# Optimization experiments

Hardware: AMD Instinct MI355X
Metric: run time of the kernel (lower is better)

The kernel has to match this reference:

```python
import jax, jax.numpy as jnp
import numpy as np

N = 100000
E = 1000000
P = 1000000
HID = 128
ROLE_VOCAB = 8
ROLE_DIM = 16
IDX_VOCAB = 1024
IDX_DIM = 8
FEAT = 14
IN_DIM = FEAT + IDX_DIM + ROLE_DIM  # 38


def setup_inputs() -> dict:
    key = jax.random.key(0)
    ks = jax.random.split(key, 20)
    s = 0.02
    return {
        "block_features": jax.random.normal(ks[0], (N, FEAT), jnp.float32),
        "role_ids": jax.random.randint(ks[1], (N,), 0, ROLE_VOCAB),
        "b2b_src": jax.random.randint(ks[2], (E,), 0, N),
        "b2b_dst": jax.random.randint(ks[3], (E,), 0, N),
        "b2b_w": jax.random.uniform(ks[4], (E,), jnp.float32),
        "p2b_block": jax.random.randint(ks[5], (P,), 0, N),
        "p2b_w": jax.random.uniform(ks[6], (P,), jnp.float32),
        "role_emb": jax.random.normal(ks[7], (ROLE_VOCAB, ROLE_DIM), jnp.float32),
        "idx_emb": jax.random.normal(ks[8], (IDX_VOCAB, IDX_DIM), jnp.float32),
        "W1": jax.random.normal(ks[9], (IN_DIM, HID), jnp.float32) * s,
        "b1": jnp.zeros((HID,), jnp.float32),
        "W2": jax.random.normal(ks[10], (HID, HID), jnp.float32) * s,
        "b2": jnp.zeros((HID,), jnp.float32),
        "M1": jax.random.normal(ks[11], (HID, HID), jnp.float32) * s,
        "mb1": jnp.zeros((HID,), jnp.float32),
        "M2": jax.random.normal(ks[12], (HID, HID), jnp.float32) * s,
        "mb2": jnp.zeros((HID,), jnp.float32),
        "ln_g": jnp.ones((HID,), jnp.float32),
        "ln_b": jnp.zeros((HID,), jnp.float32),
    }


def _layernorm(x, g, b, eps=1e-5):
    mu = jnp.mean(x, axis=-1, keepdims=True)
    var = jnp.mean(jnp.square(x - mu), axis=-1, keepdims=True)
    return (x - mu) * jax.lax.rsqrt(var + eps) * g + b


def reference(block_features, role_ids, b2b_src, b2b_dst, b2b_w, p2b_block, p2b_w,
              role_emb, idx_emb, W1, b1, W2, b2, M1, mb1, M2, mb2, ln_g, ln_b):
    n = block_features.shape[0]
    # embeddings + input MLP
    re = role_emb[role_ids]                                  # [N, 16]
    ie = idx_emb[jnp.arange(n) % IDX_VOCAB]                  # [N, 8]
    x = jnp.concatenate([block_features, re, ie], axis=-1)   # [N, 38]
    h = jax.nn.relu(x @ W1 + b1)
    emb = jax.nn.relu(h @ W2 + b2)                           # [N, HID]
    # b2b: symmetric weighted scatter-add of neighbor embeddings
    agg = jnp.zeros_like(emb)
    agg = agg.at[b2b_src].add(emb[b2b_dst] * b2b_w[:, None])
    agg = agg.at[b2b_dst].add(emb[b2b_src] * b2b_w[:, None])
    # p2b: agg[j] += emb[j] * w  ==  emb * (sum of pin weights per block)
    pw = jnp.zeros((n,), emb.dtype).at[p2b_block].add(p2b_w)
    agg = agg + emb * pw[:, None]
    # message MLP + residual + LayerNorm
    m = jax.nn.relu(agg @ M1 + mb1) @ M2 + mb2
    block_embeddings = _layernorm(emb + m, ln_g, ln_b)
    graph_embedding = jnp.mean(block_embeddings, axis=0)
    return block_embeddings, graph_embedding
```

## Files before the change

kernel.cpp:

```cpp
#include <hip/hip_runtime.h>

#define FEAT 14
#define ROLE_DIM 16
#define IDX_DIM 8
#define IN_DIM 38
#define HID 128
#define IDX_VOCAB 1024
#define BINN 128
#define NBINS_MAX 800
#define TILE_E 2048
#define CAPT 16
#define SCAP 64
#define SORT_CAP 4096

typedef __attribute__((ext_vector_type(8))) short short8;
typedef __attribute__((ext_vector_type(4))) float f32x4;
typedef __attribute__((ext_vector_type(2))) float f32x2;

__device__ __forceinline__ ushort f2bf(float f) {
    uint u = __float_as_uint(f);
    return (ushort)((u + 0x7FFFu + ((u >> 16) & 1u)) >> 16);
}
__device__ __forceinline__ float bf2f(ushort h) {
    return __uint_as_float((uint)h << 16);
}
__device__ __forceinline__ uchar f2fp8(float f) {
    return (uchar)(__builtin_amdgcn_cvt_pk_fp8_f32(f, f, 0, false) & 0xff);
}

__global__ void k_prep(const float* __restrict__ W1, const float* __restrict__ W2,
                       const float* __restrict__ M1, const float* __restrict__ M2,
                       ushort* __restrict__ W1t, ushort* __restrict__ W2t,
                       ushort* __restrict__ M1t, ushort* __restrict__ M2t)
{
    int t = blockIdx.x * 256 + threadIdx.x;
    if (t < 8192) {
        int c = t >> 6, k = t & 63;
        W1t[t] = (k < IN_DIM) ? f2bf(W1[k * HID + c]) : (ushort)0;
    } else if (t < 24576) {
        int u = t - 8192; int c = u >> 7, k = u & 127;
        W2t[u] = f2bf(W2[k * HID + c]);
    } else if (t < 40960) {
        int u = t - 24576; int c = u >> 7, k = u & 127;
        M1t[u] = f2bf(M1[k * HID + c]);
    } else if (t < 57344) {
        int u = t - 40960; int c = u >> 7, k = u & 127;
        M2t[u] = f2bf(M2[k * HID + c]);
    }
}

#define LDSA 32768

__global__ __launch_bounds__(256) void k_embed_mlp(
    const float* __restrict__ feat, const int* __restrict__ role_ids,
    const float* __restrict__ role_emb, const float* __restrict__ idx_emb,
    const ushort* __restrict__ W1t, const float* __restrict__ b1,
    const ushort* __restrict__ W2t, const float* __restrict__ b2,
    ushort* __restrict__ embh, uchar* __restrict__ embf8, int N)
{
    __shared__ char lds[49152];
    const int tid = threadIdx.x;
    const int w = tid >> 6, l = tid & 63;
    const int li = l & 15, hi = l >> 4;
    const int base = blockIdx.x * 64;

    for (int c = 0; c < 4; ++c) {
        int idx = c * 256 + tid;
        int col = idx >> 3, ch = idx & 7;
        uint4 v = *(const uint4*)(W1t + col * 64 + ch * 8);
        *(uint4*)(lds + col * 256 + ((ch * 16) ^ ((col & 7) << 4))) = v;
    }
    {
        int row = tid >> 2, kq = (tid & 3) * 16;
        int gr = base + row; if (gr >= N) gr = N - 1;
        int rid = role_ids[gr];
        float xv[16];
        #pragma unroll
        for (int j = 0; j < 16; ++j) {
            int k = kq + j;
            float v = 0.0f;
            if (k < FEAT)                 v = feat[gr * FEAT + k];
            else if (k < FEAT + ROLE_DIM) v = role_emb[rid * ROLE_DIM + (k - FEAT)];
            else if (k < IN_DIM)          v = idx_emb[(gr & (IDX_VOCAB - 1)) * IDX_DIM + (k - FEAT - ROLE_DIM)];
            xv[j] = v;
        }
        uint p[8];
        #pragma unroll
        for (int j = 0; j < 8; ++j)
            p[j] = (uint)f2bf(xv[2 * j]) | ((uint)f2bf(xv[2 * j + 1]) << 16);
        char* db = lds + LDSA + row * 256;
        int sw = (row & 7) << 4;
        *(uint4*)(db + ((kq * 2) ^ sw))      = make_uint4(p[0], p[1], p[2], p[3]);
        *(uint4*)(db + ((kq * 2 + 16) ^ sw)) = make_uint4(p[4], p[5], p[6], p[7]);
    }
    __syncthreads();

    f32x4 C[8];
    #pragma unroll
    for (int ct = 0; ct < 8; ++ct) C[ct] = (f32x4){0.f, 0.f, 0.f, 0.f};
    {
        const int arow = w * 16 + li;
        const int asw = (arow & 7) << 4;
        #pragma unroll
        for (int ks = 0; ks < 2; ++ks) {
            short8 a = *(short8*)(lds + LDSA + arow * 256 + ((ks * 64 + hi * 16) ^ asw));
            #pragma unroll
            for (int ct = 0; ct < 8; ++ct) {
                int bcol = ct * 16 + li;
                short8 b = *(short8*)(lds + bcol * 256 + ((ks * 64 + hi * 16) ^ ((bcol & 7) << 4)));
                C[ct] = __builtin_amdgcn_mfma_f32_16x16x32_bf16(a, b, C[ct], 0, 0, 0);
            }
        }
    }
    __syncthreads();

    #pragma unroll
    for (int ct = 0; ct < 8; ++ct) {
        int col = ct * 16 + li;
        float bv = b1[col];
        #pragma unroll
        for (int r = 0; r < 4; ++r) {
            int hrow = w * 16 + hi * 4 + r;
            float h = fmaxf(C[ct][r] + bv, 0.0f);
            *(ushort*)(lds + LDSA + hrow * 256 + ((col * 2) ^ ((hrow & 7) << 4))) = f2bf(h);
        }
    }
    for (int c = 0; c < 8; ++c) {
        int idx = c * 256 + tid;
        int col = idx >> 4, ch = idx & 15;
        uint4 v = *(const uint4*)(W2t + col * 128 + ch * 8);
        *(uint4*)(lds + col * 256 + ((ch * 16) ^ ((col & 7) << 4))) = v;
    }
    __syncthreads();

    f32x4 C2[8];
    #pragma unroll
    for (int ct = 0; ct < 8; ++ct) C2[ct] = (f32x4){0.f, 0.f, 0.f, 0.f};
    {
        const int arow = w * 16 + li;
        const int asw = (arow & 7) << 4;
        #pragma unroll
        for (int ks = 0; ks < 4; ++ks) {
            short8 a = *(short8*)(lds + LDSA + arow * 256 + ((ks * 64 + hi * 16) ^ asw));
            #pragma unroll
            for (int ct = 0; ct < 8; ++ct) {
                int bcol = ct * 16 + li;
                short8 b = *(short8*)(lds + bcol * 256 + ((ks * 64 + hi * 16) ^ ((bcol & 7) << 4)));
                C2[ct] = __builtin_amdgcn_mfma_f32_16x16x32_bf16(a, b, C2[ct], 0, 0, 0);
            }
        }
    }

    #pragma unroll
    for (int ct = 0; ct < 8; ++ct) {
        int col = ct * 16 + li;
        float bv = b2[col];
        #pragma unroll
        for (int r = 0; r < 4; ++r) {
            int gr = base + w * 16 + hi * 4 + r;
            if (gr < N) {
                float o = fmaxf(C2[ct][r] + bv, 0.0f);
                embh[(size_t)gr * 128 + col] = f2bf(o);
                embf8[(size_t)gr * 128 + col] = f2fp8(o);
            }
        }
    }
}

__global__ __launch_bounds__(1024) void k_binp(
    const int* __restrict__ src, const int* __restrict__ dst,
    const float* __restrict__ w, uint* __restrict__ staged,
    int* __restrict__ cnt,
    const int* __restrict__ pb, const float* __restrict__ pv,
    float* __restrict__ pw,
    int E, int P, int nbins, int chunk, int chunkP)
{
    __shared__ uint buf[NBINS_MAX * CAPT];
    __shared__ int curT[NBINS_MAX];
    __shared__ int segCur[NBINS_MAX];
    const int tid = threadIdx.x;
    const int blk = blockIdx.x;
    for (int i = tid; i < nbins; i += 1024) { curT[i] = 0; segCur[i] = 0; }
    __syncthreads();

    const int lo = blk * chunk;
    const int hiE = (lo + chunk) < E ? (lo + chunk) : E;
    for (int t0 = lo; t0 < hiE; t0 += TILE_E) {
        int t1 = t0 + TILE_E; if (t1 > hiE) t1 = hiE;
        for (int i = t0 + tid; i < t1; i += 1024) {
            int s = src[i], d = dst[i];
            uint q = (uint)(w[i] * 255.0f + 0.5f);
            int bs = s >> 7;
            uint es = ((uint)(s & 127) << 25) | ((uint)d << 8) | q;
            int ps = atomicAdd(&curT[bs], 1);
            if (ps < CAPT) buf[bs * CAPT + ps] = es;
            else { int gp = segCur[bs] + ps;
                   if (gp < SCAP) staged[((size_t)bs * 256 + blk) * SCAP + gp] = es; }
            int bd = d >> 7;
            uint ed = ((uint)(d & 127) << 25) | ((uint)s << 8) | q;
            int pd = atomicAdd(&curT[bd], 1);
            if (pd < CAPT) buf[bd * CAPT + pd] = ed;
            else { int gp = segCur[bd] + pd;
                   if (gp < SCAP) staged[((size_t)bd * 256 + blk) * SCAP + gp] = ed; }
        }
        __syncthreads();
        for (int b = tid; b < nbins; b += 1024) {
            int tot = curT[b];
            int base = segCur[b];
            int k = tot < CAPT ? tot : CAPT;
            if (base + k > SCAP) { k = SCAP - base; if (k < 0) k = 0; }
            uint* dp = staged + ((size_t)b * 256 + blk) * SCAP + base;
            for (int i = 0; i < k; ++i) dp[i] = buf[b * CAPT + i];
            segCur[b] = base + tot;
            curT[b] = 0;
        }
        __syncthreads();
    }
    for (int i = tid; i < nbins; i += 1024)
        cnt[blk * nbins + i] = segCur[i] < SCAP ? segCur[i] : SCAP;

    int loP = blk * chunkP;
    int hiP = loP + chunkP; if (hiP > P) hiP = P;
    for (int i = loP + tid; i < hiP; i += 1024)
        atomicAdd(&pw[pb[i]], pv[i]);
}

#define AREG 32768
#define WSUM 65536

__global__ __launch_bounds__(256) void k_agg_mlp(
    const uint* __restrict__ staged, const int* __restrict__ cnt,
    const ushort* __restrict__ embh, const uchar* __restrict__ embf8,
    const float* __restrict__ pw,
    const ushort* __restrict__ M1t, const ushort* __restrict__ M2t,
    const float* __restrict__ mb1, const float* __restrict__ mb2,
    const float* __restrict__ ln_g, const float* __restrict__ ln_b,
    float* __restrict__ out, float* __restrict__ gsum, int N, int nbins)
{
    __shared__ char lds[67584];
    uint* sorted  = (uint*)lds;
    int*  hist    = (int*)(lds + 16384);
    int*  startL  = (int*)(lds + 16384 + 512);
    int*  curL    = (int*)(lds + 16384 + 1024);
    int*  sc      = (int*)(lds + 16384 + 1536);

    const int tid = threadIdx.x;
    const int b = blockIdx.x;
    const int baseNode = b << 7;
    const int w = tid >> 6, l = tid & 63;
    const int li = l & 15, hi = l >> 4;

    if (tid < BINN) hist[tid] = 0;
    __syncthreads();

    const int c = cnt[tid * nbins + b];
    const uint* sp = staged + ((size_t)b * 256 + tid) * SCAP;
    for (int k = 0; k < c; ++k)
        atomicAdd(&hist[sp[k] >> 25], 1);
    __syncthreads();

    int v = (tid < BINN) ? hist[tid] : 0;
    if (tid < BINN) sc[tid] = v;
    __syncthreads();
    for (int off = 1; off < BINN; off <<= 1) {
        int u = (tid < BINN && tid >= off) ? sc[tid - off] : 0;
        __syncthreads();
        if (tid < BINN) sc[tid] += u;
        __syncthreads();
    }
    if (tid < BINN) {
        startL[tid] = sc[tid] - v;
        curL[tid]   = sc[tid] - v;
    }
    __syncthreads();

    for (int k = 0; k < c; ++k) {
        uint e = sp[k];
        int pos = atomicAdd(&curL[e >> 25], 1);
        if (pos < SORT_CAP) sorted[pos] = e;
    }
    __syncthreads();

    {
        const int g  = tid >> 3;
        const int cg = tid & 7;
        const int c0 = cg * 16;
        for (int h = 0; h < 4; ++h) {
            int nl = h * 32 + g;
            int node = baseNode + nl;
            uint p[8];
            if (node < N) {
                float acc[16];
                float pwn = pw[node];
                const uint4* r = (const uint4*)(embh + ((size_t)node << 7) + c0);
                uint4 u0 = r[0], u1 = r[1];
                uint uu[8] = {u0.x, u0.y, u0.z, u0.w, u1.x, u1.y, u1.z, u1.w};
                #pragma unroll
                for (int j = 0; j < 8; ++j) {
                    acc[2*j]   = __uint_as_float(uu[j] << 16) * pwn;
                    acc[2*j+1] = __uint_as_float(uu[j] & 0xffff0000u) * pwn;
                }
                const int st = startL[nl], deg = hist[nl];
                #pragma unroll 4
                for (int i = 0; i < deg; ++i) {
                    uint en = sorted[st + i];
                    int nb   = (int)((en >> 8) & 0x1FFFFu);
                    float wt = (float)(en & 255u) * (1.0f / 255.0f);
                    uint4 q = *(const uint4*)(embf8 + ((size_t)nb << 7) + c0);
                    uint qq[4] = {q.x, q.y, q.z, q.w};
                    #pragma unroll
                    for (int j = 0; j < 4; ++j) {
                        f32x2 lo = __builtin_amdgcn_cvt_pk_f32_fp8(qq[j], false);
                        f32x2 hi2 = __builtin_amdgcn_cvt_pk_f32_fp8(qq[j], true);
                        acc[4*j+0] = fmaf(lo.x,  wt, acc[4*j+0]);
                        acc[4*j+1] = fmaf(lo.y,  wt, acc[4*j+1]);
                        acc[4*j+2] = fmaf(hi2.x, wt, acc[4*j+2]);
                        acc[4*j+3] = fmaf(hi2.y, wt, acc[4*j+3]);
                    }
                }
                #pragma unroll
                for (int j = 0; j < 8; ++j)
                    p[j] = (uint)f2bf(acc[2*j]) | ((uint)f2bf(acc[2*j+1]) << 16);
            } else {
                #pragma unroll
                for (int j = 0; j < 8; ++j) p[j] = 0;
            }
            char* db = lds + AREG + nl * 256;
            int sw = (nl & 7) << 4;
            *(uint4*)(db + ((c0 * 2) ^ sw))      = make_uint4(p[0], p[1], p[2], p[3]);
            *(uint4*)(db + ((c0 * 2 + 16) ^ sw)) = make_uint4(p[4], p[5], p[6], p[7]);
        }
    }
    __syncthreads();

    for (int cc = 0; cc < 8; ++cc) {
        int idx = cc * 256 + tid;
        int col = idx >> 4, ch = idx & 15;
        uint4 vv = *(const uint4*)(M1t + col * 128 + ch * 8);
        *(uint4*)(lds + col * 256 + ((ch * 16) ^ ((col & 7) << 4))) = vv;
    }
    __syncthreads();

    #pragma unroll
    for (int h2 = 0; h2 < 2; ++h2) {
        f32x4 C1[8];
        #pragma unroll
        for (int ct = 0; ct < 8; ++ct) C1[ct] = (f32x4){0.f, 0.f, 0.f, 0.f};
        const int arow = h2 * 64 + w * 16 + li;
        const int asw = (arow & 7) << 4;
        #pragma unroll
        for (int ks = 0; ks < 4; ++ks) {
            short8 a = *(short8*)(lds + AREG + arow * 256 + ((ks * 64 + hi * 16) ^ asw));
            #pragma unroll
            for (int ct = 0; ct < 8; ++ct) {
                int bcol = ct * 16 + li;
                short8 bb = *(short8*)(lds + bcol * 256 + ((ks * 64 + hi * 16) ^ ((bcol & 7) << 4)));
                C1[ct] = __builtin_amdgcn_mfma_f32_16x16x32_bf16(a, bb, C1[ct], 0, 0, 0);
            }
        }
        #pragma unroll
        for (int ct = 0; ct < 8; ++ct) {
            int col = ct * 16 + li;
            float bv = mb1[col];
            #pragma unroll
            for (int r = 0; r < 4; ++r) {
                int hrow = h2 * 64 + w * 16 + hi * 4 + r;
                float h = fmaxf(C1[ct][r] + bv, 0.0f);
                *(ushort*)(lds + AREG + hrow * 256 + ((col * 2) ^ ((hrow & 7) << 4))) = f2bf(h);
            }
        }
    }
    __syncthreads();

    for (int cc = 0; cc < 8; ++cc) {
        int idx = cc * 256 + tid;
        int col = idx >> 4, ch = idx & 15;
        uint4 vv = *(const uint4*)(M2t + col * 128 + ch * 8);
        *(uint4*)(lds + col * 256 + ((ch * 16) ^ ((col & 7) << 4))) = vv;
    }
    __syncthreads();

    float cs[8];
    #pragma unroll
    for (int ct = 0; ct < 8; ++ct) cs[ct] = 0.0f;

    #pragma unroll
    for (int h2 = 0; h2 < 2; ++h2) {
        f32x4 C2[8];
        #pragma unroll
        for (int ct = 0; ct < 8; ++ct) C2[ct] = (f32x4){0.f, 0.f, 0.f, 0.f};
        const int arow = h2 * 64 + w * 16 + li;
        const int asw = (arow & 7) << 4;
        #pragma unroll
        for (int ks = 0; ks < 4; ++ks) {
            short8 a = *(short8*)(lds + AREG + arow * 256 + ((ks * 64 + hi * 16) ^ asw));
            #pragma unroll
            for (int ct = 0; ct < 8; ++ct) {
                int bcol = ct * 16 + li;
                short8 bb = *(short8*)(lds + bcol * 256 + ((ks * 64 + hi * 16) ^ ((bcol & 7) << 4)));
                C2[ct] = __builtin_amdgcn_mfma_f32_16x16x32_bf16(a, bb, C2[ct], 0, 0, 0);
            }
        }

        float y[8][4];
        #pragma unroll
        for (int ct = 0; ct < 8; ++ct) {
            int col = ct * 16 + li;
            float bv = mb2[col];
            #pragma unroll
            for (int r = 0; r < 4; ++r) {
                int gr = baseNode + h2 * 64 + w * 16 + hi * 4 + r;
                int grc = gr < N ? gr : N - 1;
                y[ct][r] = C2[ct][r] + bv + bf2f(embh[(size_t)grc * 128 + col]);
            }
        }
        float rs[4] = {0, 0, 0, 0}, rq[4] = {0, 0, 0, 0};
        #pragma unroll
        for (int ct = 0; ct < 8; ++ct)
            #pragma unroll
            for (int r = 0; r < 4; ++r) { rs[r] += y[ct][r]; rq[r] += y[ct][r] * y[ct][r]; }
        #pragma unroll
        for (int m = 1; m < 16; m <<= 1) {
            #pragma unroll
            for (int r = 0; r < 4; ++r) {
                rs[r] += __shfl_xor(rs[r], m);
                rq[r] += __shfl_xor(rq[r], m);
            }
        }
        float mu[4], rstd[4];
        #pragma unroll
        for (int r = 0; r < 4; ++r) {
            mu[r] = rs[r] * (1.0f / HID);
            float var = rq[r] * (1.0f / HID) - mu[r] * mu[r];
            rstd[r] = rsqrtf(var + 1e-5f);
        }
        #pragma unroll
        for (int ct = 0; ct < 8; ++ct) {
            int col = ct * 16 + li;
            float g = ln_g[col], bb2 = ln_b[col];
            #pragma unroll
            for (int r = 0; r < 4; ++r) {
                int gr = baseNode + h2 * 64 + w * 16 + hi * 4 + r;
                float o = (y[ct][r] - mu[r]) * rstd[r] * g + bb2;
                if (gr < N) {
                    out[(size_t)gr * 128 + col] = o;
                    cs[ct] += o;
                }
            }
        }
    }

    #pragma unroll
    for (int m = 16; m < 64; m <<= 1) {
        #pragma unroll
        for (int ct = 0; ct < 8; ++ct) cs[ct] += __shfl_xor(cs[ct], m);
    }
    float* wsum = (float*)(lds + WSUM);
    if (hi == 0) {
        #pragma unroll
        for (int ct = 0; ct < 8; ++ct) wsum[w * 128 + ct * 16 + li] = cs[ct];
    }
    __syncthreads();
    if (tid < 128) {
        float s = wsum[tid] + wsum[128 + tid] + wsum[256 + tid] + wsum[384 + tid];
        atomicAdd(&gsum[tid], s);
    }
}

__global__ void k_graph(const float* __restrict__ gsum, float* __restrict__ out,
                        int N)
{
    int j = threadIdx.x;
    out[(size_t)N * HID + j] = gsum[j] * (1.0f / (float)N);
}

extern "C" void kernel_launch(void* const* d_in, const int* in_sizes, int n_in,
                              void* d_out, int out_size, void* d_ws, size_t ws_size,
                              hipStream_t stream)
{
    const float* feat      = (const float*)d_in[0];
    const int*   role_ids  = (const int*)  d_in[1];
    const int*   b2b_src   = (const int*)  d_in[2];
    const int*   b2b_dst   = (const int*)  d_in[3];
    const float* b2b_w     = (const float*)d_in[4];
    const int*   p2b_block = (const int*)  d_in[5];
    const float* p2b_w     = (const float*)d_in[6];
    const float* role_emb  = (const float*)d_in[7];
    const float* idx_emb   = (const float*)d_in[8];
    const float* W1        = (const float*)d_in[9];
    const float* b1        = (const float*)d_in[10];
    const float* W2        = (const float*)d_in[11];
    const float* b2        = (const float*)d_in[12];
    const float* M1        = (const float*)d_in[13];
    const float* mb1       = (const float*)d_in[14];
    const float* M2        = (const float*)d_in[15];
    const float* mb2       = (const float*)d_in[16];
    const float* ln_g      = (const float*)d_in[17];
    const float* ln_b      = (const float*)d_in[18];

    const int N = in_sizes[1];
    const int E = in_sizes[2];
    const int P = in_sizes[5];

    float* out = (float*)d_out;

    const int nbins = (N + BINN - 1) >> 7;
    const int chunk  = (E + 255) / 256;
    const int chunkP = (P + 255) / 256;

    char* ws = (char*)d_ws;
    size_t embhBytes = (size_t)N * HID * sizeof(ushort);
    size_t embf8Bytes= (size_t)N * HID;
    size_t stagBytes = (size_t)nbins * 256 * SCAP * sizeof(uint);
    size_t cntBytes  = (((size_t)256 * nbins * sizeof(int)) + 15) & ~15ull;
    size_t vecBytes  = (size_t)N * sizeof(float);

    ushort* embh    = (ushort*)ws;  ws += embhBytes;
    uchar*  embf8   = (uchar*)ws;   ws += embf8Bytes;
    uint*   staged  = (uint*)ws;    ws += stagBytes;
    int*    cnt     = (int*)ws;     ws += cntBytes;
    float*  pw      = (float*)ws;   ws += vecBytes;
    float*  gsum    = (float*)ws;   ws += 512;
    ushort* W1t     = (ushort*)ws;  ws += 8192  * sizeof(ushort);
    ushort* W2t     = (ushort*)ws;  ws += 16384 * sizeof(ushort);
    ushort* M1t     = (ushort*)ws;  ws += 16384 * sizeof(ushort);
    ushort* M2t     = (ushort*)ws;  ws += 16384 * sizeof(ushort);

    hipMemsetAsync(pw, 0, vecBytes + 512, stream);

    const int nBlocks64 = (N + 63) / 64;

    k_prep<<<224, 256, 0, stream>>>(W1, W2, M1, M2, W1t, W2t, M1t, M2t);

    k_embed_mlp<<<nBlocks64, 256, 0, stream>>>(
        feat, role_ids, role_emb, idx_emb, W1t, b1, W2t, b2, embh, embf8, N);

    k_binp<<<256, 1024, 0, stream>>>(b2b_src, b2b_dst, b2b_w, staged, cnt,
                                     p2b_block, p2b_w, pw, E, P, nbins,
                                     chunk, chunkP);

    k_agg_mlp<<<nbins, 256, 0, stream>>>(
        staged, cnt, embh, embf8, pw, M1t, M2t, mb1, mb2, ln_g, ln_b,
        out, gsum, N, nbins);

    k_graph<<<1, HID, 0, stream>>>(gsum, out, N);
}
```

Baseline: 232.7 us.

## Fuse embedding MLP and edge binning into one interleaved kernel with more segments

Merges the embedding MLP kernel and the edge/pin binning kernel into a single launch. Even-numbered blocks run the embedding work and odd-numbered blocks run the binning, so the compute-bound and memory/atomic-bound phases overlap on the GPU. Binning now uses 1024 segments of 256 threads, each a single pass with a smaller per-bin LDS buffer and staging capacity, replacing 256 segments of 1024 threads that looped over tiles. The aggregation kernel now reads four segments per thread. This cuts launch gaps and improves overlap, but a lower staging cap per segment risks dropping edges when one bin gets crowded, and aggregation has to read more segments.

After: 217.6 us. -6.5%, faster.

```diff
diff --git a/kernel.cpp b/kernel.cpp
--- a/kernel.cpp
+++ b/kernel.cpp
@@ -8,9 +8,9 @@
 #define IDX_VOCAB 1024
 #define BINN 128
 #define NBINS_MAX 800
-#define TILE_E 2048
-#define CAPT 16
-#define SCAP 64
+#define NSEG 1024
+#define BINP_CAPT 8
+#define BINP_SCAP 16
 #define SORT_CAP 4096
 
 typedef __attribute__((ext_vector_type(8))) short short8;
@@ -51,18 +51,18 @@
 
 #define LDSA 32768
 
-__global__ __launch_bounds__(256) void k_embed_mlp(
+__device__ __forceinline__ void embed_body(
+    char* lds, int id,
     const float* __restrict__ feat, const int* __restrict__ role_ids,
     const float* __restrict__ role_emb, const float* __restrict__ idx_emb,
     const ushort* __restrict__ W1t, const float* __restrict__ b1,
     const ushort* __restrict__ W2t, const float* __restrict__ b2,
     ushort* __restrict__ embh, uchar* __restrict__ embf8, int N)
 {
-    __shared__ char lds[49152];
     const int tid = threadIdx.x;
     const int w = tid >> 6, l = tid & 63;
     const int li = l & 15, hi = l >> 4;
-    const int base = blockIdx.x * 64;
+    const int base = id * 64;
 
     for (int c = 0; c < 4; ++c) {
         int idx = c * 256 + tid;
@@ -167,62 +167,80 @@
     }
 }
 
-__global__ __launch_bounds__(1024) void k_binp(
+__device__ __forceinline__ void binp_body(
+    char* lds, int id,
     const int* __restrict__ src, const int* __restrict__ dst,
-    const float* __restrict__ w, uint* __restrict__ staged,
+    const float* __restrict__ wgt, uint* __restrict__ staged,
     int* __restrict__ cnt,
     const int* __restrict__ pb, const float* __restrict__ pv,
     float* __restrict__ pw,
-    int E, int P, int nbins, int chunk, int chunkP)
-{
-    __shared__ uint buf[NBINS_MAX * CAPT];
-    __shared__ int curT[NBINS_MAX];
-    __shared__ int segCur[NBINS_MAX];
+    int E, int P, int nbins, int chunkE, int chunkP)
+{
+    uint* buf   = (uint*)lds;
+    int* curT   = (int*)(lds + 25600);
+    int* segCur = (int*)(lds + 28800);
     const int tid = threadIdx.x;
-    const int blk = blockIdx.x;
-    for (int i = tid; i < nbins; i += 1024) { curT[i] = 0; segCur[i] = 0; }
-    __syncthreads();
-
-    const int lo = blk * chunk;
-    const int hiE = (lo + chunk) < E ? (lo + chunk) : E;
-    for (int t0 = lo; t0 < hiE; t0 += TILE_E) {
-        int t1 = t0 + TILE_E; if (t1 > hiE) t1 = hiE;
-        for (int i = t0 + tid; i < t1; i += 1024) {
-            int s = src[i], d = dst[i];
-            uint q = (uint)(w[i] * 255.0f + 0.5f);
-            int bs = s >> 7;
-            uint es = ((uint)(s & 127) << 25) | ((uint)d << 8) | q;
-            int ps = atomicAdd(&curT[bs], 1);
-            if (ps < CAPT) buf[bs * CAPT + ps] = es;
-            else { int gp = segCur[bs] + ps;
-                   if (gp < SCAP) staged[((size_t)bs * 256 + blk) * SCAP + gp] = es; }
-            int bd = d >> 7;
-            uint ed = ((uint)(d & 127) << 25) | ((uint)s << 8) | q;
-            int pd = atomicAdd(&curT[bd], 1);
-            if (pd < CAPT) buf[bd * CAPT + pd] = ed;
-            else { int gp = segCur[bd] + pd;
-                   if (gp < SCAP) staged[((size_t)bd * 256 + blk) * SCAP + gp] = ed; }
-        }
-        __syncthreads();
-        for (int b = tid; b < nbins; b += 1024) {
-            int tot = curT[b];
-            int base = segCur[b];
-            int k = tot < CAPT ? tot : CAPT;
-            if (base + k > SCAP) { k = SCAP - base; if (k < 0) k = 0; }
-            uint* dp = staged + ((size_t)b * 256 + blk) * SCAP + base;
-            for (int i = 0; i < k; ++i) dp[i] = buf[b * CAPT + i];
-            segCur[b] = base + tot;
-            curT[b] = 0;
-        }
-        __syncthreads();
-    }
-    for (int i = tid; i < nbins; i += 1024)
-        cnt[blk * nbins + i] = segCur[i] < SCAP ? segCur[i] : SCAP;
-
-    int loP = blk * chunkP;
+    for (int i = tid; i < nbins; i += 256) { curT[i] = 0; segCur[i] = 0; }
+    __syncthreads();
+
+    const int lo = id * chunkE;
+    const int hiE = (lo + chunkE) < E ? (lo + chunkE) : E;
+    for (int i = lo + tid; i < hiE; i += 256) {
+        int s = src[i], d = dst[i];
+        uint q = (uint)(wgt[i] * 255.0f + 0.5f);
+        int bs = s >> 7;
+        uint es = ((uint)(s & 127) << 25) | ((uint)d << 8) | q;
+        int ps = atomicAdd(&curT[bs], 1);
+        if (ps < BINP_CAPT) buf[bs * BINP_CAPT + ps] = es;
+        else if (ps < BINP_SCAP)
+            staged[((size_t)bs * NSEG + id) * BINP_SCAP + ps] = es;
+        int bd = d >> 7;
+        uint ed = ((uint)(d & 127) << 25) | ((uint)s << 8) | q;
+        int pd = atomicAdd(&curT[bd], 1);
+        if (pd < BINP_CAPT) buf[bd * BINP_CAPT + pd] = ed;
+        else if (pd < BINP_SCAP)
+            staged[((size_t)bd * NSEG + id) * BINP_SCAP + pd] = ed;
+    }
+    __syncthreads();
+    for (int b = tid; b < nbins; b += 256) {
+        int tot = curT[b];
+        int k = tot < BINP_CAPT ? tot : BINP_CAPT;
+        uint* dp = staged + ((size_t)b * NSEG + id) * BINP_SCAP;
+        for (int i = 0; i < k; ++i) dp[i] = buf[b * BINP_CAPT + i];
+        cnt[id * nbins + b] = tot < BINP_SCAP ? tot : BINP_SCAP;
+    }
+
+    int loP = id * chunkP;
     int hiP = loP + chunkP; if (hiP > P) hiP = P;
-    for (int i = loP + tid; i < hiP; i += 1024)
+    for (int i = loP + tid; i < hiP; i += 256)
         atomicAdd(&pw[pb[i]], pv[i]);
+}
+
+__global__ __launch_bounds__(256) void k_embed_binp(
+    const float* __restrict__ feat, const int* __restrict__ role_ids,
+    const float* __restrict__ role_emb, const float* __restrict__ idx_emb,
+    const ushort* __restrict__ W1t, const float* __restrict__ b1,
+    const ushort* __restrict__ W2t, const float* __restrict__ b2,
+    ushort* __restrict__ embh, uchar* __restrict__ embf8,
+    const int* __restrict__ src, const int* __restrict__ dst,
+    const float* __restrict__ wgt, uint* __restrict__ staged,
+    int* __restrict__ cnt,
+    const int* __restrict__ pb, const float* __restrict__ pv,
+    float* __restrict__ pw,
+    int N, int E, int P, int nbins, int chunkE, int chunkP)
+{
+    __shared__ char lds[49152];
+    const int bid = blockIdx.x;
+    int role, id;
+    if (bid < 2 * NSEG) { role = bid & 1; id = bid >> 1; }
+    else                { role = 0; id = NSEG + (bid - 2 * NSEG); }
+
+    if (role == 0)
+        embed_body(lds, id, feat, role_ids, role_emb, idx_emb,
+                   W1t, b1, W2t, b2, embh, embf8, N);
+    else
+        binp_body(lds, id, src, dst, wgt, staged, cnt, pb, pv, pw,
+                  E, P, nbins, chunkE, chunkP);
 }
 
 #define AREG 32768
@@ -253,10 +271,15 @@
     if (tid < BINN) hist[tid] = 0;
     __syncthreads();
 
-    const int c = cnt[tid * nbins + b];
-    const uint* sp = staged + ((size_t)b * 256 + tid) * SCAP;
-    for (int k = 0; k < c; ++k)
-        atomicAdd(&hist[sp[k] >> 25], 1);
+    int cSeg[4];
+    #pragma unroll
+    for (int ss = 0; ss < 4; ++ss) {
+        int seg = ss * 256 + tid;
+        cSeg[ss] = cnt[seg * nbins + b];
+        const uint* sp = staged + ((size_t)b * NSEG + seg) * BINP_SCAP;
+        for (int k = 0; k < cSeg[ss]; ++k)
+            atomicAdd(&hist[sp[k] >> 25], 1);
+    }
     __syncthreads();
 
     int v = (tid < BINN) ? hist[tid] : 0;
@@ -274,10 +297,15 @@
     }
     __syncthreads();
 
-    for (int k = 0; k < c; ++k) {
-        uint e = sp[k];
-        int pos = atomicAdd(&curL[e >> 25], 1);
-        if (pos < SORT_CAP) sorted[pos] = e;
+    #pragma unroll
+    for (int ss = 0; ss < 4; ++ss) {
+        int seg = ss * 256 + tid;
+        const uint* sp = staged + ((size_t)b * NSEG + seg) * BINP_SCAP;
+        for (int k = 0; k < cSeg[ss]; ++k) {
+            uint e = sp[k];
+            int pos = atomicAdd(&curL[e >> 25], 1);
+            if (pos < SORT_CAP) sorted[pos] = e;
+        }
     }
     __syncthreads();
 
@@ -505,14 +533,14 @@
     float* out = (float*)d_out;
 
     const int nbins = (N + BINN - 1) >> 7;
-    const int chunk  = (E + 255) / 256;
-    const int chunkP = (P + 255) / 256;
+    const int chunkE = (E + NSEG - 1) / NSEG;
+    const int chunkP = (P + NSEG - 1) / NSEG;
 
     char* ws = (char*)d_ws;
     size_t embhBytes = (size_t)N * HID * sizeof(ushort);
     size_t embf8Bytes= (size_t)N * HID;
-    size_t stagBytes = (size_t)nbins * 256 * SCAP * sizeof(uint);
-    size_t cntBytes  = (((size_t)256 * nbins * sizeof(int)) + 15) & ~15ull;
+    size_t stagBytes = (size_t)nbins * NSEG * BINP_SCAP * sizeof(uint);
+    size_t cntBytes  = (((size_t)NSEG * nbins * sizeof(int)) + 15) & ~15ull;
     size_t vecBytes  = (size_t)N * sizeof(float);
 
     ushort* embh    = (ushort*)ws;  ws += embhBytes;
@@ -528,16 +556,14 @@
 
     hipMemsetAsync(pw, 0, vecBytes + 512, stream);
 
-    const int nBlocks64 = (N + 63) / 64;
+    const int nEmbed = (N + 63) / 64;
 
     k_prep<<<224, 256, 0, stream>>>(W1, W2, M1, M2, W1t, W2t, M1t, M2t);
 
-    k_embed_mlp<<<nBlocks64, 256, 0, stream>>>(
-        feat, role_ids, role_emb, idx_emb, W1t, b1, W2t, b2, embh, embf8, N);
-
-    k_binp<<<256, 1024, 0, stream>>>(b2b_src, b2b_dst, b2b_w, staged, cnt,
-                                     p2b_block, p2b_w, pw, E, P, nbins,
-                                     chunk, chunkP);
+    k_embed_binp<<<nEmbed + NSEG, 256, 0, stream>>>(
+        feat, role_ids, role_emb, idx_emb, W1t, b1, W2t, b2, embh, embf8,
+        b2b_src, b2b_dst, b2b_w, staged, cnt, p2b_block, p2b_w, pw,
+        N, E, P, nbins, chunkE, chunkP);
 
     k_agg_mlp<<<nbins, 256, 0, stream>>>(
         staged, cnt, embh, embf8, pw, M1t, M2t, mb1, mb2, ln_g, ln_b,
```
